# Kernel tuning notes

Measured on AMD Instinct MI355X. Metric: run time of the kernel, lower is better.

The kernel has to match this reference:

```python
import jax, jax.numpy as jnp
import numpy as np

# dims
N, E, HID = 20000, 320000, 128
L, H = 12, 4            # num_layers, heads
C = 2 * HID             # h width = in_channels = out_channels*heads = 256
OC = C // H             # per-head out channels = 64
FF = 4 * HID            # ffn hidden = 512
LN_EPS = 1e-5
SLOPE = 0.2             # GATConv leaky_relu negative slope


def _layer_norm(x, g, b):
    m = x.mean(-1, keepdims=True)
    v = ((x - m) ** 2).mean(-1, keepdims=True)
    return (x - m) * jax.lax.rsqrt(v + LN_EPS) * g + b


def setup_inputs() -> dict:
    key = jax.random.key(0)
    ks = jax.random.split(key, 16)
    s = 0.05
    f32 = jnp.float32
    return {
        "hf": jax.random.normal(ks[0], (N, HID), f32),
        "hs": jax.random.normal(ks[1], (N, HID), f32),
        "edge_index": jax.random.randint(ks[2], (2, E), 0, N, dtype=jnp.int32),
        # GATConv params (stacked over layers)
        "W": jax.random.normal(ks[3], (L, C, H * OC), f32) * s,       # lin (no bias)
        "att_src": jax.random.normal(ks[4], (L, H, OC), f32) * s,
        "att_dst": jax.random.normal(ks[5], (L, H, OC), f32) * s,
        "gat_b": jax.random.normal(ks[6], (L, C), f32) * s,            # GATConv bias
        # FFN params
        "w1": jax.random.normal(ks[7], (L, C, FF), f32) * s,
        "b1": jax.random.normal(ks[8], (L, FF), f32) * s,
        "w2": jax.random.normal(ks[9], (L, FF, C), f32) * s,
        "b2": jax.random.normal(ks[10], (L, C), f32) * s,
        # LayerNorm params
        "ln1_g": jnp.ones((L, C), f32),
        "ln1_b": jnp.zeros((L, C), f32),
        "ln2_g": jnp.ones((L, C), f32),
        "ln2_b": jnp.zeros((L, C), f32),
    }


def reference(hf, hs, edge_index, W, att_src, att_dst, gat_b,
              w1, b1, w2, b2, ln1_g, ln1_b, ln2_g, ln2_b):
    # PyG GATConv add_self_loops=True
    loop = jnp.arange(N, dtype=edge_index.dtype)
    src = jnp.concatenate([edge_index[0], loop])  # [E+N]
    dst = jnp.concatenate([edge_index[1], loop])

    h = jnp.concatenate([hf, hs], axis=-1)  # [N, C]
    for i in range(L):
        # --- GATConv + residual + LN (dropout = identity at eval) ---
        r = h
        xh = (h @ W[i]).reshape(N, H, OC)              # [N,H,OC]
        a_s = (xh * att_src[i]).sum(-1)                # [N,H]
        a_d = (xh * att_dst[i]).sum(-1)                # [N,H]
        e = jax.nn.leaky_relu(a_s[src] + a_d[dst], SLOPE)          # [E+N,H]
        m = jax.ops.segment_max(e, dst, num_segments=N)            # [N,H]
        ex = jnp.exp(e - m[dst])
        z = jax.ops.segment_sum(ex, dst, num_segments=N)           # [N,H]
        alpha = ex / z[dst]                                        # segment softmax
        msg = xh[src] * alpha[..., None]                           # [E+N,H,OC]
        out = jax.ops.segment_sum(msg, dst, num_segments=N).reshape(N, C) + gat_b[i]
        h = _layer_norm(out + r, ln1_g[i], ln1_b[i])
        # --- FFN + residual + LN ---
        r = h
        f = jax.nn.relu(h @ w1[i] + b1[i]) @ w2[i] + b2[i]
        h = _layer_norm(f + r, ln2_g[i], ln2_b[i])

    return h[:, :HID], h[:, HID:]
```

## Files before the change

### kernel.cpp

```cpp
#include <hip/hip_runtime.h>
#include <hip/hip_bf16.h>
#include <math.h>

#define C_DIM 256
#define HID 128
#define HEADS 4
#define OC 64
#define FF_DIM 512
#define NLAYERS 12

constexpr float LN_EPS = 1e-5f;
constexpr float SLOPE  = 0.2f;

typedef __attribute__((ext_vector_type(4))) float f32x4;
typedef __attribute__((ext_vector_type(8))) short bf16x8_t;
typedef __attribute__((ext_vector_type(4))) int i32x4;

__device__ __forceinline__ float leaky(float x) { return x > 0.f ? x : SLOPE * x; }

__device__ __forceinline__ float bf2f(unsigned short u) {
    union { unsigned i; float f; } v; v.i = ((unsigned)u) << 16; return v.f;
}

__global__ void zero_i32_kernel(int* __restrict__ p, int n) {
    int i = blockIdx.x * blockDim.x + threadIdx.x;
    if (i < n) p[i] = 0;
}

__global__ void concat_kernel(const float* __restrict__ hf, const float* __restrict__ hs,
                              float* __restrict__ h, __hip_bfloat16* __restrict__ hb, int Nn) {
    int idx = blockIdx.x * blockDim.x + threadIdx.x;
    int total = Nn * C_DIM;
    if (idx < total) {
        int n = idx >> 8;
        int c = idx & 255;
        float v = (c < HID) ? hf[n * HID + c] : hs[n * HID + (c - HID)];
        h[idx] = v;
        hb[idx] = __float2bfloat16(v);
    }
}

__global__ void transp_bf16_kernel(const float* __restrict__ in,
                                   __hip_bfloat16* __restrict__ out, int K, int N) {
    __shared__ float t[32][33];
    const float* inl = in + (size_t)blockIdx.z * K * N;
    __hip_bfloat16* outl = out + (size_t)blockIdx.z * K * N;
    int kb = blockIdx.y * 32, nb = blockIdx.x * 32;
    int tx = threadIdx.x & 31, ty = threadIdx.x >> 5;
    #pragma unroll
    for (int r = 0; r < 32; r += 8)
        t[ty + r][tx] = inl[(size_t)(kb + ty + r) * N + nb + tx];
    __syncthreads();
    #pragma unroll
    for (int r = 0; r < 32; r += 8)
        outl[(size_t)(nb + ty + r) * K + kb + tx] = __float2bfloat16(t[tx][ty + r]);
}

__global__ void hist_kernel(const int* __restrict__ dst, int* __restrict__ counts, int E) {
    int e = blockIdx.x * blockDim.x + threadIdx.x;
    if (e < E) atomicAdd(&counts[dst[e]], 1);
}

__global__ void scan_kernel(const int* __restrict__ counts, int* __restrict__ offsets,
                            int* __restrict__ cursor, int n) {
    __shared__ int wsum[16];
    __shared__ int carry_s;
    const int lane = threadIdx.x & 63, wid = threadIdx.x >> 6;
    if (threadIdx.x == 0) carry_s = 0;
    __syncthreads();
    for (int base = 0; base < n; base += 1024) {
        int i = base + (int)threadIdx.x;
        int v = (i < n) ? counts[i] : 0;
        int x = v;
        #pragma unroll
        for (int off = 1; off < 64; off <<= 1) {
            int t = __shfl_up(x, off);
            if (lane >= off) x += t;
        }
        if (lane == 63) wsum[wid] = x;
        __syncthreads();
        if (threadIdx.x == 0) {
            int acc = carry_s;
            #pragma unroll
            for (int w = 0; w < 16; ++w) { int t = wsum[w]; wsum[w] = acc; acc += t; }
            carry_s = acc;
        }
        __syncthreads();
        int excl = wsum[wid] + x - v;
        if (i < n) { offsets[i] = excl; cursor[i] = excl; }
        __syncthreads();
    }
    if (threadIdx.x == 0) offsets[n] = carry_s;
}

__global__ void fill_kernel(const int* __restrict__ src, const int* __restrict__ dst,
                            int* __restrict__ cursor, int* __restrict__ csr_src,
                            int* __restrict__ csr_dst, int E) {
    int e = blockIdx.x * blockDim.x + threadIdx.x;
    if (e < E) {
        int d = dst[e];
        int p = atomicAdd(&cursor[d], 1);
        csr_src[p] = src[e];
        csr_dst[p] = d;
    }
}

__global__ void wexp_kernel(const int* __restrict__ csr, const int* __restrict__ csr_dst,
                            const float* __restrict__ a_s, const float* __restrict__ a_d,
                            float* __restrict__ wexp, int E) {
    int i = blockIdx.x * blockDim.x + threadIdx.x;
    if (i >= E) return;
    int s = csr[i], d = csr_dst[i];
    float4 av = *(const float4*)&a_s[(size_t)s * 4];
    float4 dv = *(const float4*)&a_d[(size_t)d * 4];
    float4 w;
    w.x = __expf(leaky(av.x + dv.x));
    w.y = __expf(leaky(av.y + dv.y));
    w.z = __expf(leaky(av.z + dv.z));
    w.w = __expf(leaky(av.w + dv.w));
    *(float4*)&wexp[(size_t)i * 4] = w;
}

#define GBM 64
#define GBN 64
#define GBK 64
#define GLS 72

__global__ __launch_bounds__(256) void gemm_bf16_kernel(
    const __hip_bfloat16* __restrict__ A,
    const __hip_bfloat16* __restrict__ BT,
    const float* __restrict__ bias,
    __hip_bfloat16* __restrict__ Cb,
    const float* __restrict__ attS,
    const float* __restrict__ attD,
    float* __restrict__ aS,
    float* __restrict__ aD,
    int M, int N, int K, int relu)
{
    __shared__ short As[GBM * GLS];
    __shared__ short Bs[GBN * GLS];
    __shared__ float attP[2][2][GBM];
    const int tid = threadIdx.x;
    const int wave = tid >> 6, lane = tid & 63;
    const int lr = lane & 15, lq = lane >> 4;
    const int wm = (wave >> 1) * 32, wn = (wave & 1) * 32;
    const int row0 = blockIdx.x * GBM, col0 = blockIdx.y * GBN;

    const int sr = tid >> 2;
    const int sc = (tid & 3) * 16;

    f32x4 acc[2][2] = {};

    for (int k0 = 0; k0 < K; k0 += GBK) {
        int gr = row0 + sr;
        i32x4 va0 = {}, va1 = {};
        if (gr < M) {
            const __hip_bfloat16* ap = &A[(size_t)gr * K + k0 + sc];
            va0 = *(const i32x4*)ap;
            va1 = *(const i32x4*)(ap + 8);
        }
        *(i32x4*)&As[sr * GLS + sc] = va0;
        *(i32x4*)&As[sr * GLS + sc + 8] = va1;
        const __hip_bfloat16* bp = &BT[(size_t)(col0 + sr) * K + k0 + sc];
        *(i32x4*)&Bs[sr * GLS + sc] = *(const i32x4*)bp;
        *(i32x4*)&Bs[sr * GLS + sc + 8] = *(const i32x4*)(bp + 8);
        __syncthreads();

        #pragma unroll
        for (int ks = 0; ks < 2; ++ks) {
            bf16x8_t af[2], bfr[2];
            #pragma unroll
            for (int t = 0; t < 2; ++t) {
                af[t]  = *(const bf16x8_t*)&As[(wm + t * 16 + lr) * GLS + ks * 32 + lq * 8];
                bfr[t] = *(const bf16x8_t*)&Bs[(wn + t * 16 + lr) * GLS + ks * 32 + lq * 8];
            }
            #pragma unroll
            for (int mt = 0; mt < 2; ++mt)
                #pragma unroll
                for (int nt = 0; nt < 2; ++nt)
                    acc[mt][nt] = __builtin_amdgcn_mfma_f32_16x16x32_bf16(
                        af[mt], bfr[nt], acc[mt][nt], 0, 0, 0);
        }
        __syncthreads();
    }

    float bv[2];
    #pragma unroll
    for (int nt = 0; nt < 2; ++nt)
        bv[nt] = bias ? bias[col0 + wn + nt * 16 + lr] : 0.f;

    #pragma unroll
    for (int mt = 0; mt < 2; ++mt) {
        #pragma unroll
        for (int r = 0; r < 4; ++r) {
            int grow = row0 + wm + mt * 16 + lq * 4 + r;
            if (grow >= M) continue;
            #pragma unroll
            for (int nt = 0; nt < 2; ++nt) {
                float v = acc[mt][nt][r] + bv[nt];
                if (relu) v = fmaxf(v, 0.f);
                Cb[(size_t)grow * N + col0 + wn + nt * 16 + lr] = __float2bfloat16(v);
            }
        }
    }

    if (aS) {
        const int head = col0 >> 6;
        float atS[2], atD[2];
        #pragma unroll
        for (int nt = 0; nt < 2; ++nt) {
            int c = col0 + wn + nt * 16 + lr;
            atS[nt] = attS[c];
            atD[nt] = attD[c];
        }
        #pragma unroll
        for (int mt = 0; mt < 2; ++mt) {
            #pragma unroll
            for (int r = 0; r < 4; ++r) {
                float vs = acc[mt][0][r] * atS[0] + acc[mt][1][r] * atS[1];
                float vd = acc[mt][0][r] * atD[0] + acc[mt][1][r] * atD[1];
                #pragma unroll
                for (int off = 1; off < 16; off <<= 1) {
                    vs += __shfl_xor(vs, off);
                    vd += __shfl_xor(vd, off);
                }
                if (lr == 0) {
                    int rl = wm + mt * 16 + lq * 4 + r;
                    attP[wave & 1][0][rl] = vs;
                    attP[wave & 1][1][rl] = vd;
                }
            }
        }
        __syncthreads();
        if (tid < GBM) {
            int grow = row0 + tid;
            if (grow < M) {
                aS[grow * HEADS + head] = attP[0][0][tid] + attP[1][0][tid];
                aD[grow * HEADS + head] = attP[0][1][tid] + attP[1][1][tid];
            }
        }
    }
}

__global__ __launch_bounds__(256) void agg_kernel(
    const __hip_bfloat16* __restrict__ xhb, const float* __restrict__ a_s,
    const float* __restrict__ a_d, const int* __restrict__ csr,
    const int* __restrict__ offs, const float* __restrict__ wexp,
    const float* __restrict__ gat_b, const float* __restrict__ ln_g,
    const float* __restrict__ ln_b, float* __restrict__ h,
    __hip_bfloat16* __restrict__ hb, int Nn)
{
    const int lane = threadIdx.x & 63;
    const int n = __builtin_amdgcn_readfirstlane(blockIdx.x * 4 + (threadIdx.x >> 6));
    if (n >= Nn) return;
    const int head = lane >> 4;
    const int c0 = lane * 4;
    const unsigned short* x = (const unsigned short*)xhb;

    float4 res = *(const float4*)&h[(size_t)n * C_DIM + c0];

    float wself = __expf(leaky(a_s[n * 4 + head] + a_d[n * 4 + head]));
    ushort4 xs = *(const ushort4*)&x[(size_t)n * C_DIM + c0];
    float acc0[4], acc1[4] = {}, acc2[4] = {}, acc3[4] = {};
    acc0[0] = wself * bf2f(xs.x);
    acc0[1] = wself * bf2f(xs.y);
    acc0[2] = wself * bf2f(xs.z);
    acc0[3] = wself * bf2f(xs.w);
    float z = wself;

    const int beg = offs[n], end = offs[n + 1];
    int i = beg;
    for (; i + 4 <= end; i += 4) {
        int s0 = csr[i], s1 = csr[i + 1], s2 = csr[i + 2], s3 = csr[i + 3];
        float w0 = wexp[(size_t)(i + 0) * 4 + head];
        float w1 = wexp[(size_t)(i + 1) * 4 + head];
        float w2 = wexp[(size_t)(i + 2) * 4 + head];
        float w3 = wexp[(size_t)(i + 3) * 4 + head];
        ushort4 x0 = *(const ushort4*)&x[(size_t)s0 * C_DIM + c0];
        ushort4 x1 = *(const ushort4*)&x[(size_t)s1 * C_DIM + c0];
        ushort4 x2 = *(const ushort4*)&x[(size_t)s2 * C_DIM + c0];
        ushort4 x3 = *(const ushort4*)&x[(size_t)s3 * C_DIM + c0];
        acc0[0] += w0 * bf2f(x0.x); acc0[1] += w0 * bf2f(x0.y);
        acc0[2] += w0 * bf2f(x0.z); acc0[3] += w0 * bf2f(x0.w);
        acc1[0] += w1 * bf2f(x1.x); acc1[1] += w1 * bf2f(x1.y);
        acc1[2] += w1 * bf2f(x1.z); acc1[3] += w1 * bf2f(x1.w);
        acc2[0] += w2 * bf2f(x2.x); acc2[1] += w2 * bf2f(x2.y);
        acc2[2] += w2 * bf2f(x2.z); acc2[3] += w2 * bf2f(x2.w);
        acc3[0] += w3 * bf2f(x3.x); acc3[1] += w3 * bf2f(x3.y);
        acc3[2] += w3 * bf2f(x3.z); acc3[3] += w3 * bf2f(x3.w);
        z += (w0 + w1) + (w2 + w3);
    }
    for (; i < end; ++i) {
        int s0 = csr[i];
        float w0 = wexp[(size_t)i * 4 + head];
        ushort4 x0 = *(const ushort4*)&x[(size_t)s0 * C_DIM + c0];
        acc0[0] += w0 * bf2f(x0.x); acc0[1] += w0 * bf2f(x0.y);
        acc0[2] += w0 * bf2f(x0.z); acc0[3] += w0 * bf2f(x0.w);
        z += w0;
    }

    float4 gb = *(const float4*)&gat_b[c0];
    float rz = 1.0f / z;
    float val[4];
    val[0] = (acc0[0] + acc1[0] + acc2[0] + acc3[0]) * rz + gb.x + res.x;
    val[1] = (acc0[1] + acc1[1] + acc2[1] + acc3[1]) * rz + gb.y + res.y;
    val[2] = (acc0[2] + acc1[2] + acc2[2] + acc3[2]) * rz + gb.z + res.z;
    val[3] = (acc0[3] + acc1[3] + acc2[3] + acc3[3]) * rz + gb.w + res.w;

    float s1 = (val[0] + val[1]) + (val[2] + val[3]);
    float s2 = (val[0] * val[0] + val[1] * val[1]) + (val[2] * val[2] + val[3] * val[3]);
    #pragma unroll
    for (int off = 1; off < 64; off <<= 1) {
        s1 += __shfl_xor(s1, off);
        s2 += __shfl_xor(s2, off);
    }
    float mean = s1 * (1.0f / C_DIM);
    float inv = rsqrtf(s2 * (1.0f / C_DIM) - mean * mean + LN_EPS);
    float4 g = *(const float4*)&ln_g[c0];
    float4 bb = *(const float4*)&ln_b[c0];
    float4 o;
    o.x = (val[0] - mean) * inv * g.x + bb.x;
    o.y = (val[1] - mean) * inv * g.y + bb.y;
    o.z = (val[2] - mean) * inv * g.z + bb.z;
    o.w = (val[3] - mean) * inv * g.w + bb.w;
    *(float4*)&h[(size_t)n * C_DIM + c0] = o;
    ushort4 ob;
    ob.x = __bfloat16_as_ushort(__float2bfloat16(o.x));
    ob.y = __bfloat16_as_ushort(__float2bfloat16(o.y));
    ob.z = __bfloat16_as_ushort(__float2bfloat16(o.z));
    ob.w = __bfloat16_as_ushort(__float2bfloat16(o.w));
    *(ushort4*)&((unsigned short*)hb)[(size_t)n * C_DIM + c0] = ob;
}

__global__ __launch_bounds__(256) void ln2_kernel(
    const __hip_bfloat16* __restrict__ fb, const float* __restrict__ ln_g,
    const float* __restrict__ ln_b, float* __restrict__ h,
    __hip_bfloat16* __restrict__ hb, float* __restrict__ out_split, int Nn)
{
    const int lane = threadIdx.x & 63;
    const int n = __builtin_amdgcn_readfirstlane(blockIdx.x * 4 + (threadIdx.x >> 6));
    if (n >= Nn) return;
    const int c0 = lane * 4;
    const unsigned short* f = (const unsigned short*)fb;

    float4 res = *(const float4*)&h[(size_t)n * C_DIM + c0];
    ushort4 fv = *(const ushort4*)&f[(size_t)n * C_DIM + c0];
    float val[4];
    val[0] = bf2f(fv.x) + res.x;
    val[1] = bf2f(fv.y) + res.y;
    val[2] = bf2f(fv.z) + res.z;
    val[3] = bf2f(fv.w) + res.w;

    float s1 = (val[0] + val[1]) + (val[2] + val[3]);
    float s2 = (val[0] * val[0] + val[1] * val[1]) + (val[2] * val[2] + val[3] * val[3]);
    #pragma unroll
    for (int off = 1; off < 64; off <<= 1) {
        s1 += __shfl_xor(s1, off);
        s2 += __shfl_xor(s2, off);
    }
    float mean = s1 * (1.0f / C_DIM);
    float inv = rsqrtf(s2 * (1.0f / C_DIM) - mean * mean + LN_EPS);
    float4 g = *(const float4*)&ln_g[c0];
    float4 bb = *(const float4*)&ln_b[c0];
    float4 o;
    o.x = (val[0] - mean) * inv * g.x + bb.x;
    o.y = (val[1] - mean) * inv * g.y + bb.y;
    o.z = (val[2] - mean) * inv * g.z + bb.z;
    o.w = (val[3] - mean) * inv * g.w + bb.w;

    if (out_split) {
        size_t off_ = (c0 < HID) ? ((size_t)n * HID + c0)
                                 : ((size_t)Nn * HID + (size_t)n * HID + (c0 - HID));
        *(float4*)&out_split[off_] = o;
    } else {
        *(float4*)&h[(size_t)n * C_DIM + c0] = o;
        ushort4 ob;
        ob.x = __bfloat16_as_ushort(__float2bfloat16(o.x));
        ob.y = __bfloat16_as_ushort(__float2bfloat16(o.y));
        ob.z = __bfloat16_as_ushort(__float2bfloat16(o.z));
        ob.w = __bfloat16_as_ushort(__float2bfloat16(o.w));
        *(ushort4*)&((unsigned short*)hb)[(size_t)n * C_DIM + c0] = ob;
    }
}

extern "C" void kernel_launch(void* const* d_in, const int* in_sizes, int n_in,
                              void* d_out, int out_size, void* d_ws, size_t ws_size,
                              hipStream_t stream)
{
    const float* hf       = (const float*)d_in[0];
    const float* hs       = (const float*)d_in[1];
    const int*   edge     = (const int*)  d_in[2];
    const float* W        = (const float*)d_in[3];
    const float* att_src  = (const float*)d_in[4];
    const float* att_dst  = (const float*)d_in[5];
    const float* gat_b    = (const float*)d_in[6];
    const float* w1       = (const float*)d_in[7];
    const float* b1       = (const float*)d_in[8];
    const float* w2       = (const float*)d_in[9];
    const float* b2       = (const float*)d_in[10];
    const float* ln1g     = (const float*)d_in[11];
    const float* ln1b     = (const float*)d_in[12];
    const float* ln2g     = (const float*)d_in[13];
    const float* ln2b     = (const float*)d_in[14];
    float* out = (float*)d_out;

    const int N = in_sizes[0] / HID;
    const int E = in_sizes[2] / 2;
    const int* e_src = edge;
    const int* e_dst = edge + E;

    char* p = (char*)d_ws;
    auto alloc = [&](size_t bytes) {
        char* r = p;
        p += (bytes + 255) & ~(size_t)255;
        return (void*)r;
    };
    float*          h      = (float*)alloc((size_t)N * C_DIM * 4);
    __hip_bfloat16* hb     = (__hip_bfloat16*)alloc((size_t)N * C_DIM * 2);
    __hip_bfloat16* xhb    = (__hip_bfloat16*)alloc((size_t)N * C_DIM * 2);
    __hip_bfloat16* fbuf   = (__hip_bfloat16*)alloc((size_t)N * C_DIM * 2);
    __hip_bfloat16* midb   = (__hip_bfloat16*)alloc((size_t)N * FF_DIM * 2);
    float*          a_s    = (float*)alloc((size_t)N * HEADS * 4);
    float*          a_d    = (float*)alloc((size_t)N * HEADS * 4);
    float*          wexp   = (float*)alloc((size_t)E * HEADS * 4);
    int*            counts = (int*)alloc((size_t)N * 4);
    int*            offs   = (int*)alloc((size_t)(N + 1) * 4);
    int*            cursor = (int*)alloc((size_t)N * 4);
    int*            csr    = (int*)alloc((size_t)E * 4);
    int*            csrd   = (int*)alloc((size_t)E * 4);
    __hip_bfloat16* WT     = (__hip_bfloat16*)alloc((size_t)NLAYERS * C_DIM * C_DIM * 2);
    __hip_bfloat16* w1T    = (__hip_bfloat16*)alloc((size_t)NLAYERS * C_DIM * FF_DIM * 2);
    __hip_bfloat16* w2T    = (__hip_bfloat16*)alloc((size_t)NLAYERS * FF_DIM * C_DIM * 2);

    {
        int total = N * C_DIM;
        concat_kernel<<<(total + 255) / 256, 256, 0, stream>>>(hf, hs, h, hb, N);
    }
    transp_bf16_kernel<<<dim3(C_DIM / 32, C_DIM / 32, NLAYERS), 256, 0, stream>>>(W, WT, C_DIM, C_DIM);
    transp_bf16_kernel<<<dim3(FF_DIM / 32, C_DIM / 32, NLAYERS), 256, 0, stream>>>(w1, w1T, C_DIM, FF_DIM);
    transp_bf16_kernel<<<dim3(C_DIM / 32, FF_DIM / 32, NLAYERS), 256, 0, stream>>>(w2, w2T, FF_DIM, C_DIM);

    zero_i32_kernel<<<(N + 255) / 256, 256, 0, stream>>>(counts, N);
    hist_kernel<<<(E + 255) / 256, 256, 0, stream>>>(e_dst, counts, E);
    scan_kernel<<<1, 1024, 0, stream>>>(counts, offs, cursor, N);
    fill_kernel<<<(E + 255) / 256, 256, 0, stream>>>(e_src, e_dst, cursor, csr, csrd, E);

    const int gm = (N + GBM - 1) / GBM;

    for (int l = 0; l < NLAYERS; ++l) {
        const __hip_bfloat16* Wl  = WT  + (size_t)l * C_DIM * C_DIM;
        const __hip_bfloat16* w1l = w1T + (size_t)l * C_DIM * FF_DIM;
        const __hip_bfloat16* w2l = w2T + (size_t)l * FF_DIM * C_DIM;
        const float* asl  = att_src + (size_t)l * C_DIM;
        const float* adl  = att_dst + (size_t)l * C_DIM;
        const float* gbl  = gat_b + (size_t)l * C_DIM;
        const float* b1l  = b1 + (size_t)l * FF_DIM;
        const float* b2l  = b2 + (size_t)l * C_DIM;
        const float* g1l  = ln1g + (size_t)l * C_DIM;
        const float* be1l = ln1b + (size_t)l * C_DIM;
        const float* g2l  = ln2g + (size_t)l * C_DIM;
        const float* be2l = ln2b + (size_t)l * C_DIM;

        gemm_bf16_kernel<<<dim3(gm, C_DIM / GBN), 256, 0, stream>>>(
            hb, Wl, nullptr, xhb, asl, adl, a_s, a_d, N, C_DIM, C_DIM, 0);
        wexp_kernel<<<(E + 255) / 256, 256, 0, stream>>>(csr, csrd, a_s, a_d, wexp, E);
        agg_kernel<<<(N + 3) / 4, 256, 0, stream>>>(
            xhb, a_s, a_d, csr, offs, wexp, gbl, g1l, be1l, h, hb, N);
        gemm_bf16_kernel<<<dim3(gm, FF_DIM / GBN), 256, 0, stream>>>(
            hb, w1l, b1l, midb, nullptr, nullptr, nullptr, nullptr,
            N, FF_DIM, C_DIM, 1);
        gemm_bf16_kernel<<<dim3(gm, C_DIM / GBN), 256, 0, stream>>>(
            midb, w2l, b2l, fbuf, nullptr, nullptr, nullptr, nullptr,
            N, C_DIM, FF_DIM, 0);
        ln2_kernel<<<(N + 3) / 4, 256, 0, stream>>>(
            fbuf, g2l, be2l, h, hb, (l == NLAYERS - 1) ? out : nullptr, N);
    }
}
```

Before: 1.300 ms.

## Fuse edge softmax weights into aggregation and split edges across half-waves

Removes the separate per-edge exp-weight kernel and its E×4 float buffer (and the csr_dst array), computing each edge's exp(leaky(a_s+a_d)) inside the aggregation loop instead. Each wave now splits a node's edge list between two 32-lane halves that each load 16-byte bf16 chunks and then combine partial sums via a cross-half shuffle. This trades one extra kernel launch and its global write/read traffic for some redundant exp work per lane and a gather of a_s per edge. Only the lower half writes the LayerNorm output.

```diff
diff --git a/kernel.cpp b/kernel.cpp
--- a/kernel.cpp
+++ b/kernel.cpp
@@ -20,6 +20,16 @@
 
 __device__ __forceinline__ float bf2f(unsigned short u) {
     union { unsigned i; float f; } v; v.i = ((unsigned)u) << 16; return v.f;
+}
+__device__ __forceinline__ void bf2x(unsigned u, float& lo, float& hi) {
+    union { unsigned i; float f; } a, b;
+    a.i = u << 16; b.i = u & 0xffff0000u;
+    lo = a.f; hi = b.f;
+}
+__device__ __forceinline__ unsigned packbf(float lo, float hi) {
+    unsigned a = __bfloat16_as_ushort(__float2bfloat16(lo));
+    unsigned b = __bfloat16_as_ushort(__float2bfloat16(hi));
+    return a | (b << 16);
 }
 
 __global__ void zero_i32_kernel(int* __restrict__ p, int n) {
@@ -94,31 +104,13 @@
 }
 
 __global__ void fill_kernel(const int* __restrict__ src, const int* __restrict__ dst,
-                            int* __restrict__ cursor, int* __restrict__ csr_src,
-                            int* __restrict__ csr_dst, int E) {
+                            int* __restrict__ cursor, int* __restrict__ csr_src, int E) {
     int e = blockIdx.x * blockDim.x + threadIdx.x;
     if (e < E) {
         int d = dst[e];
         int p = atomicAdd(&cursor[d], 1);
         csr_src[p] = src[e];
-        csr_dst[p] = d;
-    }
-}
-
-__global__ void wexp_kernel(const int* __restrict__ csr, const int* __restrict__ csr_dst,
-                            const float* __restrict__ a_s, const float* __restrict__ a_d,
-                            float* __restrict__ wexp, int E) {
-    int i = blockIdx.x * blockDim.x + threadIdx.x;
-    if (i >= E) return;
-    int s = csr[i], d = csr_dst[i];
-    float4 av = *(const float4*)&a_s[(size_t)s * 4];
-    float4 dv = *(const float4*)&a_d[(size_t)d * 4];
-    float4 w;
-    w.x = __expf(leaky(av.x + dv.x));
-    w.y = __expf(leaky(av.y + dv.y));
-    w.z = __expf(leaky(av.z + dv.z));
-    w.w = __expf(leaky(av.w + dv.w));
-    *(float4*)&wexp[(size_t)i * 4] = w;
+    }
 }
 
 #define GBM 64
@@ -245,91 +237,136 @@
 __global__ __launch_bounds__(256) void agg_kernel(
     const __hip_bfloat16* __restrict__ xhb, const float* __restrict__ a_s,
     const float* __restrict__ a_d, const int* __restrict__ csr,
-    const int* __restrict__ offs, const float* __restrict__ wexp,
-    const float* __restrict__ gat_b, const float* __restrict__ ln_g,
-    const float* __restrict__ ln_b, float* __restrict__ h,
-    __hip_bfloat16* __restrict__ hb, int Nn)
+    const int* __restrict__ offs, const float* __restrict__ gat_b,
+    const float* __restrict__ ln_g, const float* __restrict__ ln_b,
+    float* __restrict__ h, __hip_bfloat16* __restrict__ hb, int Nn)
 {
     const int lane = threadIdx.x & 63;
     const int n = __builtin_amdgcn_readfirstlane(blockIdx.x * 4 + (threadIdx.x >> 6));
     if (n >= Nn) return;
-    const int head = lane >> 4;
-    const int c0 = lane * 4;
-    const unsigned short* x = (const unsigned short*)xhb;
-
-    float4 res = *(const float4*)&h[(size_t)n * C_DIM + c0];
-
-    float wself = __expf(leaky(a_s[n * 4 + head] + a_d[n * 4 + head]));
-    ushort4 xs = *(const ushort4*)&x[(size_t)n * C_DIM + c0];
-    float acc0[4], acc1[4] = {}, acc2[4] = {}, acc3[4] = {};
-    acc0[0] = wself * bf2f(xs.x);
-    acc0[1] = wself * bf2f(xs.y);
-    acc0[2] = wself * bf2f(xs.z);
-    acc0[3] = wself * bf2f(xs.w);
-    float z = wself;
+    const int half = lane >> 5;
+    const int sl = lane & 31;
+    const int head = sl >> 3;
+    const int c0 = sl * 8;
+    const unsigned* x = (const unsigned*)xhb;
+    const size_t rowp = (size_t)n * (C_DIM / 2) + (c0 >> 1);
+
+    const float ad = a_d[n * 4 + head];
 
     const int beg = offs[n], end = offs[n + 1];
-    int i = beg;
-    for (; i + 4 <= end; i += 4) {
-        int s0 = csr[i], s1 = csr[i + 1], s2 = csr[i + 2], s3 = csr[i + 3];
-        float w0 = wexp[(size_t)(i + 0) * 4 + head];
-        float w1 = wexp[(size_t)(i + 1) * 4 + head];
-        float w2 = wexp[(size_t)(i + 2) * 4 + head];
-        float w3 = wexp[(size_t)(i + 3) * 4 + head];
-        ushort4 x0 = *(const ushort4*)&x[(size_t)s0 * C_DIM + c0];
-        ushort4 x1 = *(const ushort4*)&x[(size_t)s1 * C_DIM + c0];
-        ushort4 x2 = *(const ushort4*)&x[(size_t)s2 * C_DIM + c0];
-        ushort4 x3 = *(const ushort4*)&x[(size_t)s3 * C_DIM + c0];
-        acc0[0] += w0 * bf2f(x0.x); acc0[1] += w0 * bf2f(x0.y);
-        acc0[2] += w0 * bf2f(x0.z); acc0[3] += w0 * bf2f(x0.w);
-        acc1[0] += w1 * bf2f(x1.x); acc1[1] += w1 * bf2f(x1.y);
-        acc1[2] += w1 * bf2f(x1.z); acc1[3] += w1 * bf2f(x1.w);
-        acc2[0] += w2 * bf2f(x2.x); acc2[1] += w2 * bf2f(x2.y);
-        acc2[2] += w2 * bf2f(x2.z); acc2[3] += w2 * bf2f(x2.w);
-        acc3[0] += w3 * bf2f(x3.x); acc3[1] += w3 * bf2f(x3.y);
-        acc3[2] += w3 * bf2f(x3.z); acc3[3] += w3 * bf2f(x3.w);
+    const int ne = end - beg;
+    const int nh0 = (ne + 1) >> 1;
+    int ih  = half ? (beg + nh0) : beg;
+    int cnt = half ? (ne - nh0) : nh0;
+
+    float acc[8] = {};
+    float z = 0.f;
+
+    {
+        float wself = __expf(leaky(a_s[n * 4 + head] + ad));
+        if (half) {
+            i32x4 xv = *(const i32x4*)&x[rowp];
+            #pragma unroll
+            for (int q = 0; q < 4; ++q) {
+                float lo, hi; bf2x((unsigned)xv[q], lo, hi);
+                acc[2 * q]     = wself * lo;
+                acc[2 * q + 1] = wself * hi;
+            }
+            z = wself;
+        }
+    }
+
+    for (; cnt >= 4; cnt -= 4, ih += 4) {
+        int s0 = csr[ih], s1 = csr[ih + 1], s2 = csr[ih + 2], s3 = csr[ih + 3];
+        float w0 = __expf(leaky(a_s[s0 * 4 + head] + ad));
+        float w1 = __expf(leaky(a_s[s1 * 4 + head] + ad));
+        float w2 = __expf(leaky(a_s[s2 * 4 + head] + ad));
+        float w3 = __expf(leaky(a_s[s3 * 4 + head] + ad));
+        i32x4 x0 = *(const i32x4*)&x[(size_t)s0 * (C_DIM / 2) + (c0 >> 1)];
+        i32x4 x1 = *(const i32x4*)&x[(size_t)s1 * (C_DIM / 2) + (c0 >> 1)];
+        i32x4 x2 = *(const i32x4*)&x[(size_t)s2 * (C_DIM / 2) + (c0 >> 1)];
+        i32x4 x3 = *(const i32x4*)&x[(size_t)s3 * (C_DIM / 2) + (c0 >> 1)];
+        #pragma unroll
+        for (int q = 0; q < 4; ++q) {
+            float lo, hi;
+            bf2x((unsigned)x0[q], lo, hi);
+            acc[2 * q] += w0 * lo; acc[2 * q + 1] += w0 * hi;
+            bf2x((unsigned)x1[q], lo, hi);
+            acc[2 * q] += w1 * lo; acc[2 * q + 1] += w1 * hi;
+            bf2x((unsigned)x2[q], lo, hi);
+            acc[2 * q] += w2 * lo; acc[2 * q + 1] += w2 * hi;
+            bf2x((unsigned)x3[q], lo, hi);
+            acc[2 * q] += w3 * lo; acc[2 * q + 1] += w3 * hi;
+        }
         z += (w0 + w1) + (w2 + w3);
     }
-    for (; i < end; ++i) {
-        int s0 = csr[i];
-        float w0 = wexp[(size_t)i * 4 + head];
-        ushort4 x0 = *(const ushort4*)&x[(size_t)s0 * C_DIM + c0];
-        acc0[0] += w0 * bf2f(x0.x); acc0[1] += w0 * bf2f(x0.y);
-        acc0[2] += w0 * bf2f(x0.z); acc0[3] += w0 * bf2f(x0.w);
+    for (; cnt > 0; --cnt, ++ih) {
+        int s0 = csr[ih];
+        float w0 = __expf(leaky(a_s[s0 * 4 + head] + ad));
+        i32x4 x0 = *(const i32x4*)&x[(size_t)s0 * (C_DIM / 2) + (c0 >> 1)];
+        #pragma unroll
+        for (int q = 0; q < 4; ++q) {
+            float lo, hi; bf2x((unsigned)x0[q], lo, hi);
+            acc[2 * q] += w0 * lo; acc[2 * q + 1] += w0 * hi;
+        }
         z += w0;
     }
 
-    float4 gb = *(const float4*)&gat_b[c0];
+    #pragma unroll
+    for (int j = 0; j < 8; ++j) acc[j] += __shfl_xor(acc[j], 32);
+    z += __shfl_xor(z, 32);
+
+    float4 res0 = *(const float4*)&h[(size_t)n * C_DIM + c0];
+    float4 res1 = *(const float4*)&h[(size_t)n * C_DIM + c0 + 4];
+    float4 gb0 = *(const float4*)&gat_b[c0];
+    float4 gb1 = *(const float4*)&gat_b[c0 + 4];
     float rz = 1.0f / z;
-    float val[4];
-    val[0] = (acc0[0] + acc1[0] + acc2[0] + acc3[0]) * rz + gb.x + res.x;
-    val[1] = (acc0[1] + acc1[1] + acc2[1] + acc3[1]) * rz + gb.y + res.y;
-    val[2] = (acc0[2] + acc1[2] + acc2[2] + acc3[2]) * rz + gb.z + res.z;
-    val[3] = (acc0[3] + acc1[3] + acc2[3] + acc3[3]) * rz + gb.w + res.w;
-
-    float s1 = (val[0] + val[1]) + (val[2] + val[3]);
-    float s2 = (val[0] * val[0] + val[1] * val[1]) + (val[2] * val[2] + val[3] * val[3]);
+    float val[8];
+    val[0] = acc[0] * rz + gb0.x + res0.x;
+    val[1] = acc[1] * rz + gb0.y + res0.y;
+    val[2] = acc[2] * rz + gb0.z + res0.z;
+    val[3] = acc[3] * rz + gb0.w + res0.w;
+    val[4] = acc[4] * rz + gb1.x + res1.x;
+    val[5] = acc[5] * rz + gb1.y + res1.y;
+    val[6] = acc[6] * rz + gb1.z + res1.z;
+    val[7] = acc[7] * rz + gb1.w + res1.w;
+
+    float s1 = 0.f, s2 = 0.f;
+    #pragma unroll
+    for (int j = 0; j < 8; ++j) { s1 += val[j]; s2 += val[j] * val[j]; }
     #pragma unroll
     for (int off = 1; off < 64; off <<= 1) {
         s1 += __shfl_xor(s1, off);
         s2 += __shfl_xor(s2, off);
     }
-    float mean = s1 * (1.0f / C_DIM);
-    float inv = rsqrtf(s2 * (1.0f / C_DIM) - mean * mean + LN_EPS);
-    float4 g = *(const float4*)&ln_g[c0];
-    float4 bb = *(const float4*)&ln_b[c0];
-    float4 o;
-    o.x = (val[0] - mean) * inv * g.x + bb.x;
-    o.y = (val[1] - mean) * inv * g.y + bb.y;
-    o.z = (val[2] - mean) * inv * g.z + bb.z;
-    o.w = (val[3] - mean) * inv * g.w + bb.w;
-    *(float4*)&h[(size_t)n * C_DIM + c0] = o;
-    ushort4 ob;
-    ob.x = __bfloat16_as_ushort(__float2bfloat16(o.x));
-    ob.y = __bfloat16_as_ushort(__float2bfloat16(o.y));
-    ob.z = __bfloat16_as_ushort(__float2bfloat16(o.z));
-    ob.w = __bfloat16_as_ushort(__float2bfloat16(o.w));
-    *(ushort4*)&((unsigned short*)hb)[(size_t)n * C_DIM + c0] = ob;
+    float mean = s1 * (1.0f / (2 * C_DIM));
+    float inv = rsqrtf(s2 * (1.0f / (2 * C_DIM)) - mean * mean + LN_EPS);
+
+    if (half == 0) {
+        float4 g0 = *(const float4*)&ln_g[c0];
+        float4 g1 = *(const float4*)&ln_g[c0 + 4];
+        float4 bb0 = *(const float4*)&ln_b[c0];
+        float4 bb1 = *(const float4*)&ln_b[c0 + 4];
+        float o[8];
+        o[0] = (val[0] - mean) * inv * g0.x + bb0.x;
+        o[1] = (val[1] - mean) * inv * g0.y + bb0.y;
+        o[2] = (val[2] - mean) * inv * g0.z + bb0.z;
+        o[3] = (val[3] - mean) * inv * g0.w + bb0.w;
+        o[4] = (val[4] - mean) * inv * g1.x + bb1.x;
+        o[5] = (val[5] - mean) * inv * g1.y + bb1.y;
+        o[6] = (val[6] - mean) * inv * g1.z + bb1.z;
+        o[7] = (val[7] - mean) * inv * g1.w + bb1.w;
+        float4 o0 = {o[0], o[1], o[2], o[3]};
+        float4 o1 = {o[4], o[5], o[6], o[7]};
+        *(float4*)&h[(size_t)n * C_DIM + c0] = o0;
+        *(float4*)&h[(size_t)n * C_DIM + c0 + 4] = o1;
+        i32x4 ob;
+        ob[0] = (int)packbf(o[0], o[1]);
+        ob[1] = (int)packbf(o[2], o[3]);
+        ob[2] = (int)packbf(o[4], o[5]);
+        ob[3] = (int)packbf(o[6], o[7]);
+        *(i32x4*)&((unsigned*)hb)[rowp] = ob;
+    }
 }
 
 __global__ __launch_bounds__(256) void ln2_kernel(
@@ -422,12 +459,10 @@
     __hip_bfloat16* midb   = (__hip_bfloat16*)alloc((size_t)N * FF_DIM * 2);
     float*          a_s    = (float*)alloc((size_t)N * HEADS * 4);
     float*          a_d    = (float*)alloc((size_t)N * HEADS * 4);
-    float*          wexp   = (float*)alloc((size_t)E * HEADS * 4);
     int*            counts = (int*)alloc((size_t)N * 4);
     int*            offs   = (int*)alloc((size_t)(N + 1) * 4);
     int*            cursor = (int*)alloc((size_t)N * 4);
     int*            csr    = (int*)alloc((size_t)E * 4);
-    int*            csrd   = (int*)alloc((size_t)E * 4);
     __hip_bfloat16* WT     = (__hip_bfloat16*)alloc((size_t)NLAYERS * C_DIM * C_DIM * 2);
     __hip_bfloat16* w1T    = (__hip_bfloat16*)alloc((size_t)NLAYERS * C_DIM * FF_DIM * 2);
     __hip_bfloat16* w2T    = (__hip_bfloat16*)alloc((size_t)NLAYERS * FF_DIM * C_DIM * 2);
@@ -443,7 +478,7 @@
     zero_i32_kernel<<<(N + 255) / 256, 256, 0, stream>>>(counts, N);
     hist_kernel<<<(E + 255) / 256, 256, 0, stream>>>(e_dst, counts, E);
     scan_kernel<<<1, 1024, 0, stream>>>(counts, offs, cursor, N);
-    fill_kernel<<<(E + 255) / 256, 256, 0, stream>>>(e_src, e_dst, cursor, csr, csrd, E);
+    fill_kernel<<<(E + 255) / 256, 256, 0, stream>>>(e_src, e_dst, cursor, csr, E);
 
     const int gm = (N + GBM - 1) / GBM;
 
@@ -463,9 +498,8 @@
 
         gemm_bf16_kernel<<<dim3(gm, C_DIM / GBN), 256, 0, stream>>>(
             hb, Wl, nullptr, xhb, asl, adl, a_s, a_d, N, C_DIM, C_DIM, 0);
-        wexp_kernel<<<(E + 255) / 256, 256, 0, stream>>>(csr, csrd, a_s, a_d, wexp, E);
         agg_kernel<<<(N + 3) / 4, 256, 0, stream>>>(
-            xhb, a_s, a_d, csr, offs, wexp, gbl, g1l, be1l, h, hb, N);
+            xhb, a_s, a_d, csr, offs, gbl, g1l, be1l, h, hb, N);
         gemm_bf16_kernel<<<dim3(gm, FF_DIM / GBN), 256, 0, stream>>>(
             hb, w1l, b1l, midb, nullptr, nullptr, nullptr, nullptr,
             N, FF_DIM, C_DIM, 1);
```

Result: faster. 1.264 ms (-2.7%).
